# Performance work log

Hardware: AMD Instinct MI355X
Metric: run time of the kernel (lower is better)

The kernel has to match this reference:

```python
import jax, jax.numpy as jnp
import numpy as np

jax.config.update("jax_enable_x64", True)  # faithful int64 fixed-point requantize

B, K, N = 2048, 4096, 8192
INT32_MAX_MINUS = 2147418112  # threshold from multiply_by_quantize_mul


def setup_inputs() -> dict:
    key = jax.random.key(0)
    k1, k2, k3 = jax.random.split(key, 3)
    x = jax.random.randint(k1, (B, K), -128, 128, dtype=jnp.int8)
    weights = jax.random.randint(k2, (N, K), -128, 128, dtype=jnp.int8)
    bias = jax.random.randint(k3, (N, 1), -1024, 1024, dtype=jnp.int32)
    return {
        "x": x,
        "weights": weights,
        "bias": bias,
        "q_mantissa": 1431655765,   # ~2/3 in Q31 fixed point
        "exponent": -3,
        "output_zero_point": -5,
    }


def multiply_by_quantize_mul(x, q_mantissa, exponent):
    # Python precedence in original: (q_mantissa + (1<<15)) >> 16
    reduced_mantissa = ((q_mantissa + (1 << 15)) >> 16) if q_mantissa < INT32_MAX_MINUS else 32767
    total_shifts = 15 - exponent
    x = x * np.int64(reduced_mantissa)
    x = x + np.int64(1 << (total_shifts - 1))  # rounding term
    return jnp.right_shift(x, total_shifts)    # arithmetic shift on signed int64


def reference(x, weights, bias, q_mantissa, exponent, output_zero_point):
    # int8 GEMM accumulated in int32: result[b, n] = sum_k x[b, k] * w[n, k]
    acc = jnp.einsum("bk,nk->bn", x.astype(jnp.int32), weights.astype(jnp.int32))
    acc = acc + bias.T  # bias [N,1] -> [1,N], broadcast over batch
    acc = multiply_by_quantize_mul(acc.astype(jnp.int64), q_mantissa, exponent)
    acc = acc + np.int64(output_zero_point)
    out = jnp.clip(acc, -128, 127).astype(jnp.int8)
    return out
```

## Files before the change

kernel.cpp:

```cpp
#include <hip/hip_runtime.h>

#define DEVI __device__ __forceinline__

typedef int i32x4 __attribute__((ext_vector_type(4)));

static constexpr int Bdim = 2048;
static constexpr int Kdim = 4096;
static constexpr int Ndim = 8192;
static constexpr int BK   = 64;
static constexpr int NT   = Kdim / BK;

typedef __attribute__((address_space(1))) const unsigned int gas_t;
typedef __attribute__((address_space(3))) unsigned int las_t;

DEVI void gload_lds16(const void* g, void* l) {
    __builtin_amdgcn_global_load_lds((gas_t*)g, (las_t*)l, 16, 0, 0);
}

DEVI int pack4(i32x4 v) {
    return (v[0] & 255) | ((v[1] & 255) << 8) | ((v[2] & 255) << 16) | (v[3] << 24);
}

__global__ void pack_i32_to_i8(const int* __restrict__ in, char* __restrict__ out, int n16) {
    int i = blockIdx.x * blockDim.x + threadIdx.x;
    if (i >= n16) return;
    const i32x4* src = (const i32x4*)in + (size_t)i * 4;
    i32x4 r;
    r[0] = pack4(src[0]);
    r[1] = pack4(src[1]);
    r[2] = pack4(src[2]);
    r[3] = pack4(src[3]);
    ((i32x4*)out)[i] = r;
}

#define CFENCE asm volatile("" ::: "memory")
DEVI void bar() { CFENCE; __builtin_amdgcn_s_barrier(); CFENCE; }
#define WAITVM(N) asm volatile("s_waitcnt vmcnt(" #N ")" ::: "memory")
#define SCHB __builtin_amdgcn_sched_barrier(0)
#define PRIO1 __builtin_amdgcn_s_setprio(1)
#define PRIO0 __builtin_amdgcn_s_setprio(0)

#define QUADH(MB)                                                                \
    do {                                                                         \
        _Pragma("unroll") for (int mm = 0; mm < 4; ++mm)                         \
        _Pragma("unroll") for (int n = 0; n < 4; ++n)                            \
            acc[(MB) + mm][n] = __builtin_amdgcn_mfma_i32_16x16x64_i8(           \
                a[(MB) + mm], b[n], acc[(MB) + mm][n], 0, 0, 0);                 \
    } while (0)

#define LDAH(MB)                                                                 \
    _Pragma("unroll") for (int mm = 0; mm < 4; ++mm)                             \
        a[(MB) + mm] = smem4[cb + a_rd16 + ((MB) + mm) * 64]

__attribute__((amdgpu_waves_per_eu(2, 2)))
__global__ __launch_bounds__(512, 2)
void gemm14(const char* __restrict__ A8, const char* __restrict__ B8,
            const int* __restrict__ bias,
            const int* __restrict__ qm_p, const int* __restrict__ ex_p,
            const int* __restrict__ zp_p, int* __restrict__ out) {
    __shared__ i32x4 smem4[6144];
    char* smem = (char*)smem4;

    const int tid  = threadIdx.x;
    const int wid  = tid >> 6;
    const int lane = tid & 63;
    const int l15  = lane & 15;
    const int lks  = lane >> 4;
    const int wr   = wid >> 2;
    const int wc   = wid & 3;

    const int bid = blockIdx.x;
    const int swz = (bid & 7) * 32 + (bid >> 3);
    const int bm  = swz >> 5;
    const int bn  = swz & 31;
    const int arow0 = bm * 256;
    const int brow0 = bn * 256;

    const int swsel = lks ^ ((l15 >> 1) & 3);
    const int a_rd16 = (wr * 128 + l15) * 4 + swsel;
    const int b_rd16 = 1024 + (wc * 64 + l15) * 4 + swsel;

    const int st_c = (tid & 3) ^ ((tid >> 3) & 3);
    const char* agp = A8 + (size_t)(arow0 + (tid >> 2)) * Kdim + st_c * 16;
    const char* bgp = B8 + (size_t)(brow0 + (tid >> 2)) * Kdim + st_c * 16;

    auto stage = [&](int t) {
        const int lb = (t % 3) * 32768 + tid * 16;
        const size_t ko = (size_t)t * BK;
        gload_lds16(agp + ko,                      &smem[lb]);
        gload_lds16(agp + ko + (size_t)128 * Kdim, &smem[lb + 8192]);
        gload_lds16(bgp + ko,                      &smem[lb + 16384]);
        gload_lds16(bgp + ko + (size_t)128 * Kdim, &smem[lb + 24576]);
    };

    i32x4 acc[8][4] = {};

    stage(0);
    stage(1);
    WAITVM(4);
    bar();

    for (int t = 0; t < NT; ++t) {
        const int cb = (t % 3) * 2048;
        if (t + 2 < NT) stage(t + 2);
        i32x4 a[8], b[4];
#pragma unroll
        for (int n = 0; n < 4; ++n) b[n] = smem4[cb + b_rd16 + n * 64];
        if (wr == 0) {
            LDAH(0);
            PRIO1; QUADH(0); PRIO0;
            SCHB;
            LDAH(4);
            PRIO1; QUADH(4); PRIO0;
        } else {
            LDAH(4);
            PRIO1; QUADH(4); PRIO0;
            SCHB;
            LDAH(0);
            PRIO1; QUADH(0); PRIO0;
        }
        if (t + 2 < NT) { WAITVM(4); }
        else            { WAITVM(0); }
        bar();
    }

    const int qm = *qm_p;
    const int ex = *ex_p;
    const int zp = *zp_p;
    const int rm = (qm < 2147418112) ? ((qm + (1 << 15)) >> 16) : 32767;
    const int shifts = 15 - ex;
    const long long rnd = (shifts > 0) ? (1LL << (shifts - 1)) : 0;

    int bv[4];
#pragma unroll
    for (int n = 0; n < 4; ++n) bv[n] = bias[brow0 + wc * 64 + n * 16 + l15];

#pragma unroll
    for (int m = 0; m < 8; ++m) {
        const int row0 = arow0 + wr * 128 + m * 16 + lks * 4;
#pragma unroll
        for (int n = 0; n < 4; ++n) {
            const int col = brow0 + wc * 64 + n * 16 + l15;
#pragma unroll
            for (int j = 0; j < 4; ++j) {
                long long v = (long long)(acc[m][n][j] + bv[n]) * rm + rnd;
                v >>= shifts;
                v += zp;
                v = v < -128 ? -128 : (v > 127 ? 127 : v);
                out[(size_t)(row0 + j) * Ndim + col] = (int)v;
            }
        }
    }
}

extern "C" void kernel_launch(void* const* d_in, const int* in_sizes, int n_in,
                              void* d_out, int out_size, void* d_ws, size_t ws_size,
                              hipStream_t stream) {
    const int* x32  = (const int*)d_in[0];
    const int* w32  = (const int*)d_in[1];
    const int* bias = (const int*)d_in[2];
    const int* qm   = (const int*)d_in[3];
    const int* ex   = (const int*)d_in[4];
    const int* zp   = (const int*)d_in[5];
    int* out = (int*)d_out;

    char* xa = (char*)d_ws;
    char* wa = xa + (size_t)Bdim * Kdim;
    const int nx16 = Bdim * Kdim / 16;
    const int nw16 = Ndim * Kdim / 16;
    pack_i32_to_i8<<<(nx16 + 255) / 256, 256, 0, stream>>>(x32, xa, nx16);
    pack_i32_to_i8<<<(nw16 + 255) / 256, 256, 0, stream>>>(w32, wa, nw16);

    const int grid = (Bdim / 256) * (Ndim / 256);
    gemm14<<<grid, 512, 0, stream>>>(xa, wa, bias, qm, ex, zp, out);
}
```

Measured before the change: 106.5 us.

## Quad-buffer LDS and double-buffer register fragments across K tiles

Grows the LDS ring from three to four stages and prefetches the next tile's A/B fragments into a second register set while the MFMAs for the current tile run. The aim is to hide LDS read latency behind matrix math. The change drops the per-wave-row half split, the sched barriers and the staggered ordering. The extra registers (24 more i32x4 fragments) and larger LDS footprint risk spilling or lowering occupancy under the 2-waves-per-EU bound.

```diff
diff --git a/kernel.cpp b/kernel.cpp
--- a/kernel.cpp
+++ b/kernel.cpp
@@ -36,29 +36,32 @@
 #define CFENCE asm volatile("" ::: "memory")
 DEVI void bar() { CFENCE; __builtin_amdgcn_s_barrier(); CFENCE; }
 #define WAITVM(N) asm volatile("s_waitcnt vmcnt(" #N ")" ::: "memory")
-#define SCHB __builtin_amdgcn_sched_barrier(0)
 #define PRIO1 __builtin_amdgcn_s_setprio(1)
 #define PRIO0 __builtin_amdgcn_s_setprio(0)
 
-#define QUADH(MB)                                                                \
+#define MFMA32(A, B)                                                             \
     do {                                                                         \
-        _Pragma("unroll") for (int mm = 0; mm < 4; ++mm)                         \
+        _Pragma("unroll") for (int mm = 0; mm < 8; ++mm)                         \
         _Pragma("unroll") for (int n = 0; n < 4; ++n)                            \
-            acc[(MB) + mm][n] = __builtin_amdgcn_mfma_i32_16x16x64_i8(           \
-                a[(MB) + mm], b[n], acc[(MB) + mm][n], 0, 0, 0);                 \
+            acc[mm][n] = __builtin_amdgcn_mfma_i32_16x16x64_i8(                  \
+                (A)[mm], (B)[n], acc[mm][n], 0, 0, 0);                           \
     } while (0)
 
-#define LDAH(MB)                                                                 \
-    _Pragma("unroll") for (int mm = 0; mm < 4; ++mm)                             \
-        a[(MB) + mm] = smem4[cb + a_rd16 + ((MB) + mm) * 64]
+#define LDFR(A, B, CB)                                                           \
+    do {                                                                         \
+        _Pragma("unroll") for (int mm = 0; mm < 8; ++mm)                         \
+            (A)[mm] = smem4[(CB) + a_rd16 + mm * 64];                            \
+        _Pragma("unroll") for (int n = 0; n < 4; ++n)                            \
+            (B)[n] = smem4[(CB) + b_rd16 + n * 64];                              \
+    } while (0)
 
 __attribute__((amdgpu_waves_per_eu(2, 2)))
 __global__ __launch_bounds__(512, 2)
-void gemm14(const char* __restrict__ A8, const char* __restrict__ B8,
+void gemm15(const char* __restrict__ A8, const char* __restrict__ B8,
             const int* __restrict__ bias,
             const int* __restrict__ qm_p, const int* __restrict__ ex_p,
             const int* __restrict__ zp_p, int* __restrict__ out) {
-    __shared__ i32x4 smem4[6144];
+    __shared__ i32x4 smem4[8192];
     char* smem = (char*)smem4;
 
     const int tid  = threadIdx.x;
@@ -84,8 +87,8 @@
     const char* agp = A8 + (size_t)(arow0 + (tid >> 2)) * Kdim + st_c * 16;
     const char* bgp = B8 + (size_t)(brow0 + (tid >> 2)) * Kdim + st_c * 16;
 
-    auto stage = [&](int t) {
-        const int lb = (t % 3) * 32768 + tid * 16;
+    auto stage = [&](int t, int cb) {
+        const int lb = cb * 16 + tid * 16;
         const size_t ko = (size_t)t * BK;
         gload_lds16(agp + ko,                      &smem[lb]);
         gload_lds16(agp + ko + (size_t)128 * Kdim, &smem[lb + 8192]);
@@ -94,34 +97,27 @@
     };
 
     i32x4 acc[8][4] = {};
+    i32x4 A0[8], B0[4], A1[8], B1[4];
 
-    stage(0);
-    stage(1);
+    stage(0, 0); stage(1, 2048); stage(2, 4096);
     WAITVM(4);
     bar();
+    int c0 = 0, c1 = 2048, c2 = 4096, c3 = 6144;
+    LDFR(A0, B0, c0);
 
-    for (int t = 0; t < NT; ++t) {
-        const int cb = (t % 3) * 2048;
-        if (t + 2 < NT) stage(t + 2);
-        i32x4 a[8], b[4];
-#pragma unroll
-        for (int n = 0; n < 4; ++n) b[n] = smem4[cb + b_rd16 + n * 64];
-        if (wr == 0) {
-            LDAH(0);
-            PRIO1; QUADH(0); PRIO0;
-            SCHB;
-            LDAH(4);
-            PRIO1; QUADH(4); PRIO0;
-        } else {
-            LDAH(4);
-            PRIO1; QUADH(4); PRIO0;
-            SCHB;
-            LDAH(0);
-            PRIO1; QUADH(0); PRIO0;
-        }
-        if (t + 2 < NT) { WAITVM(4); }
-        else            { WAITVM(0); }
+    for (int t = 0; t < NT; t += 2) {
+        if (t + 1 < NT) LDFR(A1, B1, c1);
+        if (t + 3 < NT) stage(t + 3, c3);
+        PRIO1; MFMA32(A0, B0); PRIO0;
+        if (t + 3 < NT) { WAITVM(4); } else { WAITVM(0); }
         bar();
+        if (t + 2 < NT) LDFR(A0, B0, c2);
+        if (t + 4 < NT) stage(t + 4, c0);
+        PRIO1; MFMA32(A1, B1); PRIO0;
+        if (t + 4 < NT) { WAITVM(4); } else { WAITVM(0); }
+        bar();
+        const int u0 = c0, u1 = c1;
+        c0 = c2; c1 = c3; c2 = u0; c3 = u1;
     }
 
     const int qm = *qm_p;
@@ -172,5 +168,5 @@
     pack_i32_to_i8<<<(nw16 + 255) / 256, 256, 0, stream>>>(w32, wa, nw16);
 
     const int grid = (Bdim / 256) * (Ndim / 256);
-    gemm14<<<grid, 512, 0, stream>>>(xa, wa, bias, qm, ex, zp, out);
+    gemm15<<<grid, 512, 0, stream>>>(xa, wa, bias, qm, ex, zp, out);
 }
```

New measurement: 104.6 us. No clear change (-1.8%).

## Fuse int32-to-int8 packing into GEMM main loop via register staging

Applied to the files above, without the earlier changes.

Removes the two separate pack kernels and has the GEMM read the int32 inputs directly. Each tile is loaded into registers, packed to int8, and written to LDS while the MFMAs of the current tile run. The old direct global-to-LDS loads are replaced by register staging, and the block-to-tile mapping changes. The cost is that every GEMM block now re-reads four times as many bytes of int32 input, and register use rises, which may lower occupancy.

```diff
diff --git a/kernel.cpp b/kernel.cpp
--- a/kernel.cpp
+++ b/kernel.cpp
@@ -10,56 +10,23 @@
 static constexpr int BK   = 64;
 static constexpr int NT   = Kdim / BK;
 
-typedef __attribute__((address_space(1))) const unsigned int gas_t;
-typedef __attribute__((address_space(3))) unsigned int las_t;
-
-DEVI void gload_lds16(const void* g, void* l) {
-    __builtin_amdgcn_global_load_lds((gas_t*)g, (las_t*)l, 16, 0, 0);
-}
+#define CFENCE asm volatile("" ::: "memory")
+DEVI void bar() { CFENCE; __builtin_amdgcn_s_barrier(); CFENCE; }
+#define WAITLG0 asm volatile("s_waitcnt lgkmcnt(0)" ::: "memory")
+#define PRIO1 __builtin_amdgcn_s_setprio(1)
+#define PRIO0 __builtin_amdgcn_s_setprio(0)
 
 DEVI int pack4(i32x4 v) {
     return (v[0] & 255) | ((v[1] & 255) << 8) | ((v[2] & 255) << 16) | (v[3] << 24);
 }
 
-__global__ void pack_i32_to_i8(const int* __restrict__ in, char* __restrict__ out, int n16) {
-    int i = blockIdx.x * blockDim.x + threadIdx.x;
-    if (i >= n16) return;
-    const i32x4* src = (const i32x4*)in + (size_t)i * 4;
-    i32x4 r;
-    r[0] = pack4(src[0]);
-    r[1] = pack4(src[1]);
-    r[2] = pack4(src[2]);
-    r[3] = pack4(src[3]);
-    ((i32x4*)out)[i] = r;
-}
-
-#define CFENCE asm volatile("" ::: "memory")
-DEVI void bar() { CFENCE; __builtin_amdgcn_s_barrier(); CFENCE; }
-#define WAITVM(N) asm volatile("s_waitcnt vmcnt(" #N ")" ::: "memory")
-#define SCHB __builtin_amdgcn_sched_barrier(0)
-#define PRIO1 __builtin_amdgcn_s_setprio(1)
-#define PRIO0 __builtin_amdgcn_s_setprio(0)
-
-#define QUADH(MB)                                                                \
-    do {                                                                         \
-        _Pragma("unroll") for (int mm = 0; mm < 4; ++mm)                         \
-        _Pragma("unroll") for (int n = 0; n < 4; ++n)                            \
-            acc[(MB) + mm][n] = __builtin_amdgcn_mfma_i32_16x16x64_i8(           \
-                a[(MB) + mm], b[n], acc[(MB) + mm][n], 0, 0, 0);                 \
-    } while (0)
-
-#define LDAH(MB)                                                                 \
-    _Pragma("unroll") for (int mm = 0; mm < 4; ++mm)                             \
-        a[(MB) + mm] = smem4[cb + a_rd16 + ((MB) + mm) * 64]
-
 __attribute__((amdgpu_waves_per_eu(2, 2)))
-__global__ __launch_bounds__(512, 2)
-void gemm14(const char* __restrict__ A8, const char* __restrict__ B8,
-            const int* __restrict__ bias,
-            const int* __restrict__ qm_p, const int* __restrict__ ex_p,
-            const int* __restrict__ zp_p, int* __restrict__ out) {
+__global__ __launch_bounds__(512, 1)
+void gemmf(const int* __restrict__ X32, const int* __restrict__ W32,
+           const int* __restrict__ bias, const int* __restrict__ qm_p,
+           const int* __restrict__ ex_p, const int* __restrict__ zp_p,
+           int* __restrict__ out) {
     __shared__ i32x4 smem4[6144];
-    char* smem = (char*)smem4;
 
     const int tid  = threadIdx.x;
     const int wid  = tid >> 6;
@@ -70,9 +37,8 @@
     const int wc   = wid & 3;
 
     const int bid = blockIdx.x;
-    const int swz = (bid & 7) * 32 + (bid >> 3);
-    const int bm  = swz >> 5;
-    const int bn  = swz & 31;
+    const int bm  = (bid >> 3) & 7;
+    const int bn  = (bid & 7) * 4 + (bid >> 6);
     const int arow0 = bm * 256;
     const int brow0 = bn * 256;
 
@@ -80,47 +46,68 @@
     const int a_rd16 = (wr * 128 + l15) * 4 + swsel;
     const int b_rd16 = 1024 + (wc * 64 + l15) * 4 + swsel;
 
-    const int st_c = (tid & 3) ^ ((tid >> 3) & 3);
-    const char* agp = A8 + (size_t)(arow0 + (tid >> 2)) * Kdim + st_c * 16;
-    const char* bgp = B8 + (size_t)(brow0 + (tid >> 2)) * Kdim + st_c * 16;
+    const int ra = tid >> 1, h = tid & 1;
+    const int xr  = (ra >> 1) & 3;
+    const int sl0 = (2 * h + 0) ^ xr;
+    const int sl1 = (2 * h + 1) ^ xr;
+    const i32x4* xsrc = (const i32x4*)(X32 + (size_t)(arow0 + ra) * Kdim + h * 32);
+    const i32x4* wsrc = (const i32x4*)(W32 + (size_t)(brow0 + ra) * Kdim + h * 32);
 
-    auto stage = [&](int t) {
-        const int lb = (t % 3) * 32768 + tid * 16;
-        const size_t ko = (size_t)t * BK;
-        gload_lds16(agp + ko,                      &smem[lb]);
-        gload_lds16(agp + ko + (size_t)128 * Kdim, &smem[lb + 8192]);
-        gload_lds16(bgp + ko,                      &smem[lb + 16384]);
-        gload_lds16(bgp + ko + (size_t)128 * Kdim, &smem[lb + 24576]);
+    auto loadRaw = [&](int t, i32x4* rx, i32x4* rw) {
+        const i32x4* sx = xsrc + (size_t)t * 16;
+        const i32x4* sw = wsrc + (size_t)t * 16;
+#pragma unroll
+        for (int j = 0; j < 8; ++j) { rx[j] = sx[j]; rw[j] = sw[j]; }
+    };
+    auto packTo = [&](const i32x4* rx, const i32x4* rw, i32x4* pc) {
+#pragma unroll
+        for (int c = 0; c < 2; ++c) {
+            i32x4 pa, pb;
+#pragma unroll
+            for (int q = 0; q < 4; ++q) {
+                pa[q] = pack4(rx[c * 4 + q]);
+                pb[q] = pack4(rw[c * 4 + q]);
+            }
+            pc[c] = pa; pc[2 + c] = pb;
+        }
+    };
+    auto writeLds = [&](int buf, const i32x4* pc) {
+        const int bb = buf * 2048;
+        smem4[bb + ra * 4 + sl0]        = pc[0];
+        smem4[bb + ra * 4 + sl1]        = pc[1];
+        smem4[bb + 1024 + ra * 4 + sl0] = pc[2];
+        smem4[bb + 1024 + ra * 4 + sl1] = pc[3];
     };
 
     i32x4 acc[8][4] = {};
+    i32x4 rx[8], rw[8], pc[4];
 
-    stage(0);
-    stage(1);
-    WAITVM(4);
+    loadRaw(0, rx, rw);
+    packTo(rx, rw, pc);
+    writeLds(0, pc);
+    loadRaw(1, rx, rw);
+    WAITLG0;
     bar();
 
     for (int t = 0; t < NT; ++t) {
         const int cb = (t % 3) * 2048;
-        if (t + 2 < NT) stage(t + 2);
-        i32x4 a[8], b[4];
+        i32x4 A[8], B[4];
 #pragma unroll
-        for (int n = 0; n < 4; ++n) b[n] = smem4[cb + b_rd16 + n * 64];
-        if (wr == 0) {
-            LDAH(0);
-            PRIO1; QUADH(0); PRIO0;
-            SCHB;
-            LDAH(4);
-            PRIO1; QUADH(4); PRIO0;
-        } else {
-            LDAH(4);
-            PRIO1; QUADH(4); PRIO0;
-            SCHB;
-            LDAH(0);
-            PRIO1; QUADH(0); PRIO0;
-        }
-        if (t + 2 < NT) { WAITVM(4); }
-        else            { WAITVM(0); }
+        for (int n = 0; n < 4; ++n) B[n] = smem4[cb + b_rd16 + n * 64];
+#pragma unroll
+        for (int m = 0; m < 8; ++m) A[m] = smem4[cb + a_rd16 + m * 64];
+        if (t + 1 < NT) packTo(rx, rw, pc);
+        PRIO1;
+#pragma unroll
+        for (int m = 0; m < 8; ++m)
+#pragma unroll
+            for (int n = 0; n < 4; ++n)
+                acc[m][n] = __builtin_amdgcn_mfma_i32_16x16x64_i8(
+                    A[m], B[n], acc[m][n], 0, 0, 0);
+        PRIO0;
+        if (t + 1 < NT) writeLds((t + 1) % 3, pc);
+        if (t + 2 < NT) loadRaw(t + 2, rx, rw);
+        WAITLG0;
         bar();
     }
 
@@ -164,13 +151,6 @@
     const int* zp   = (const int*)d_in[5];
     int* out = (int*)d_out;
 
-    char* xa = (char*)d_ws;
-    char* wa = xa + (size_t)Bdim * Kdim;
-    const int nx16 = Bdim * Kdim / 16;
-    const int nw16 = Ndim * Kdim / 16;
-    pack_i32_to_i8<<<(nx16 + 255) / 256, 256, 0, stream>>>(x32, xa, nx16);
-    pack_i32_to_i8<<<(nw16 + 255) / 256, 256, 0, stream>>>(w32, wa, nw16);
-
     const int grid = (Bdim / 256) * (Ndim / 256);
-    gemm14<<<grid, 512, 0, stream>>>(xa, wa, bias, qm, ex, zp, out);
+    gemmf<<<grid, 512, 0, stream>>>(x32, w32, bias, qm, ex, zp, out);
 }
```

Result: slower. 340.4 us (+219.5%).
